# Optimization experiments

Measured on AMD Instinct MI355X. Metric: run time of the kernel, lower is better.

## Reference

```python
import jax, jax.numpy as jnp
import numpy as np

NUM_GROUPS = 8
EPS = 1e-5


def setup_inputs() -> dict:
    key = jax.random.key(0)
    ks = jax.random.split(key, 4)
    C = 128
    x = jax.random.normal(ks[0], (4, C, 64, 64), dtype=jnp.float32)
    gn_weight = jnp.ones((C,), dtype=jnp.float32)
    gn_bias = jnp.zeros((C,), dtype=jnp.float32)
    qkv_weight = jax.random.normal(ks[1], (3 * C, C), dtype=jnp.float32) * (C ** -0.5)
    qkv_bias = jnp.zeros((3 * C,), dtype=jnp.float32)
    proj_weight = jax.random.normal(ks[2], (C, C), dtype=jnp.float32) * (C ** -0.5)
    proj_bias = jnp.zeros((C,), dtype=jnp.float32)
    return {
        "x": x,
        "gn_weight": gn_weight,
        "gn_bias": gn_bias,
        "qkv_weight": qkv_weight,
        "qkv_bias": qkv_bias,
        "proj_weight": proj_weight,
        "proj_bias": proj_bias,
    }


def reference(x, gn_weight, gn_bias, qkv_weight, qkv_bias, proj_weight, proj_bias):
    b, c, h, w = x.shape
    scale = c ** (-0.5)

    # GroupNorm(8, c): normalize over (channels_in_group, h, w)
    xg = x.reshape(b, NUM_GROUPS, c // NUM_GROUPS, h, w)
    mean = jnp.mean(xg, axis=(2, 3, 4), keepdims=True)
    var = jnp.var(xg, axis=(2, 3, 4), keepdims=True)
    xn = ((xg - mean) * jax.lax.rsqrt(var + EPS)).reshape(b, c, h, w)
    xn = xn * gn_weight[None, :, None, None] + gn_bias[None, :, None, None]

    # 1x1 conv QKV == channel matmul; flatten spatial to sequence n = h*w
    xn_flat = xn.reshape(b, c, h * w)  # [b, c, n]
    qkv = jnp.einsum('oc,bcn->bno', qkv_weight, xn_flat) + qkv_bias  # [b, n, 3c]
    q, k, v = qkv[..., :c], qkv[..., c:2 * c], qkv[..., 2 * c:]

    # attention: materializes [b, n, n] scores as in original
    attn = jnp.einsum('bnc,bmc->bnm', q, k) * scale
    attn = jax.nn.softmax(attn, axis=-1)
    out = jnp.einsum('bnm,bmc->bnc', attn, v)  # [b, n, c]

    # proj 1x1 conv + residual
    out = jnp.einsum('oc,bnc->bno', proj_weight, out) + proj_bias  # [b, n, c]
    out = out.transpose(0, 2, 1).reshape(b, c, h, w)
    return x + out
```

## Files before the change

### kernel.cpp

```cpp
#include <hip/hip_runtime.h>

#define BATCH 4
#define CCH 128
#define NSP 4096
#define NGRP 8
#define GROUP_ELEMS 65536
#define QSCALE 0.12751744f
#define EPS_GN 1e-5f
#define OPSTRIDE 2097152
#define LPSTRIDE 16384

typedef short s8b __attribute__((ext_vector_type(8)));
typedef float f32x4 __attribute__((ext_vector_type(4)));

static __device__ __forceinline__ short f2bf(float f) {
  union { float f; unsigned u; } v; v.f = f;
  unsigned r = (v.u + 0x7FFFu + ((v.u >> 16) & 1u)) >> 16;
  return (short)r;
}

static __device__ __forceinline__ float bf2f(short s) {
  unsigned u = ((unsigned)(unsigned short)s) << 16;
  float f; __builtin_memcpy(&f, &u, 4); return f;
}

static __device__ __forceinline__ float fexp2(float x) {
#if __has_builtin(__builtin_amdgcn_exp2f)
  return __builtin_amdgcn_exp2f(x);
#else
  return exp2f(x);
#endif
}

static __device__ __forceinline__ unsigned pack2bf(float a, float b) {
  unsigned ua, ub;
  __builtin_memcpy(&ua, &a, 4); __builtin_memcpy(&ub, &b, 4);
  ua += 0x8000u; ub += 0x8000u;
#if __has_builtin(__builtin_amdgcn_perm)
  return __builtin_amdgcn_perm(ub, ua, 0x07060302u);
#else
  return (ua >> 16) | (ub & 0xFFFF0000u);
#endif
}

static __device__ __forceinline__ f32x4 mfma16(s8b a, s8b b, f32x4 c) {
  return __builtin_amdgcn_mfma_f32_16x16x32_bf16(a, b, c, 0, 0, 0);
}

static __device__ __forceinline__ void async16(const void* g, void* l) {
  __builtin_amdgcn_global_load_lds(
      (const __attribute__((address_space(1))) void*)g,
      (__attribute__((address_space(3))) void*)l, 16, 0, 0);
}

__global__ void gn_stats(const float* __restrict__ x, float* __restrict__ part) {
  int bx = blockIdx.x;
  int ch = bx & 7, bg = bx >> 3;
  const float* base = x + (size_t)bg * GROUP_ELEMS + (size_t)ch * 8192;
  int t = threadIdx.x;
  float s = 0.f, ss = 0.f;
  #pragma unroll
  for (int i = 0; i < 8; ++i) {
    float4 v = *(const float4*)(base + i * 1024 + t * 4);
    s  += v.x + v.y + v.z + v.w;
    ss += v.x * v.x + v.y * v.y + v.z * v.z + v.w * v.w;
  }
  #pragma unroll
  for (int off = 1; off < 64; off <<= 1) {
    s  += __shfl_xor(s, off);
    ss += __shfl_xor(ss, off);
  }
  __shared__ float red[8];
  int w = t >> 6;
  if ((t & 63) == 0) { red[w * 2] = s; red[w * 2 + 1] = ss; }
  __syncthreads();
  if (t == 0) {
    part[bx * 2]     = red[0] + red[2] + red[4] + red[6];
    part[bx * 2 + 1] = red[1] + red[3] + red[5] + red[7];
  }
}

__global__ void gn_apply(const float* __restrict__ x, const float* __restrict__ gw,
                         const float* __restrict__ gb, const float* __restrict__ part,
                         short* __restrict__ xn) {
  int bx = blockIdx.x;
  int ns = bx & 7, g = (bx >> 3) & 7, b = bx >> 6;
  int bg = b * NGRP + g;
  float s = 0.f, ss = 0.f;
  #pragma unroll
  for (int j = 0; j < 8; ++j) {
    s  += part[(bg * 8 + j) * 2];
    ss += part[(bg * 8 + j) * 2 + 1];
  }
  float mean = s * (1.f / GROUP_ELEMS);
  float var  = ss * (1.f / GROUP_ELEMS) - mean * mean;
  float inv  = rsqrtf(var + EPS_GN);
  int t = threadIdx.x;
  int cl = t & 15, n4 = t >> 4;
  int c = g * 16 + cl;
  float ga = gw[c] * inv;
  float be = gb[c] - mean * ga;
  const float* xr = x + (size_t)(b * CCH + c) * NSP;
  short* xo = xn + (size_t)b * NSP * CCH + c;
  #pragma unroll
  for (int i = 0; i < 8; ++i) {
    int n = ns * 512 + i * 64 + n4 * 4;
    float4 v = *(const float4*)(xr + n);
    xo[(size_t)(n + 0) * CCH] = f2bf(v.x * ga + be);
    xo[(size_t)(n + 1) * CCH] = f2bf(v.y * ga + be);
    xo[(size_t)(n + 2) * CCH] = f2bf(v.z * ga + be);
    xo[(size_t)(n + 3) * CCH] = f2bf(v.w * ga + be);
  }
}

__global__ void qkv_gemm(const short* __restrict__ xn, const float* __restrict__ Wqkv,
                         const float* __restrict__ bias, short* __restrict__ q,
                         short* __restrict__ k, short* __restrict__ vt) {
  __shared__ short Xl[128 * 136];
  __shared__ short Wl[64 * 136];
  int bx = blockIdx.x;
  int t = threadIdx.x;
  int lane = t & 63, w = t >> 6, l15 = lane & 15, quad = lane >> 4;
  if (bx < 1024) {
    int ot = bx & 3, nt = (bx >> 2) & 63, b = bx >> 8;
    for (int idx = t; idx < 64 * 16; idx += 256) {
      int row = idx >> 4, c8 = idx & 15;
      *(s8b*)&Xl[row * 136 + c8 * 8] =
          *(const s8b*)(xn + ((size_t)(b * NSP + nt * 64 + row)) * CCH + c8 * 8);
    }
    for (int idx = t; idx < 64 * 16; idx += 256) {
      int row = idx >> 4, c8 = idx & 15;
      const float* src = Wqkv + (size_t)(ot * 64 + row) * CCH + c8 * 8;
      s8b wv;
      #pragma unroll
      for (int j = 0; j < 8; ++j) wv[j] = f2bf(src[j]);
      *(s8b*)&Wl[row * 136 + c8 * 8] = wv;
    }
    __syncthreads();
    s8b a[4];
    #pragma unroll
    for (int kc = 0; kc < 4; ++kc)
      a[kc] = *(const s8b*)&Xl[(w * 16 + l15) * 136 + kc * 32 + quad * 8];
    #pragma unroll
    for (int o4 = 0; o4 < 4; ++o4) {
      f32x4 acc = {0.f, 0.f, 0.f, 0.f};
      #pragma unroll
      for (int kc = 0; kc < 4; ++kc) {
        s8b bw = *(const s8b*)&Wl[(o4 * 16 + l15) * 136 + kc * 32 + quad * 8];
        acc = mfma16(a[kc], bw, acc);
      }
      int obase = ot * 64 + o4 * 16;
      short* dst = (obase < 128) ? q : k;
      float mulf = (obase < 128) ? QSCALE : 1.0f;
      int oc = obase - ((obase < 128) ? 0 : 128) + l15;
      float bs = bias[obase + l15];
      #pragma unroll
      for (int r = 0; r < 4; ++r) {
        int n = nt * 64 + w * 16 + quad * 4 + r;
        dst[((size_t)(b * NSP + n)) * CCH + oc] = f2bf((acc[r] + bs) * mulf);
      }
    }
  } else {
    int vbx = bx - 1024;
    int ot = vbx & 1, nt = (vbx >> 1) & 31, b = vbx >> 6;
    for (int idx = t; idx < 128 * 16; idx += 256) {
      int row = idx >> 4, c8 = idx & 15;
      *(s8b*)&Xl[row * 136 + c8 * 8] =
          *(const s8b*)(xn + ((size_t)(b * NSP + nt * 128 + row)) * CCH + c8 * 8);
    }
    for (int idx = t; idx < 64 * 16; idx += 256) {
      int row = idx >> 4, c8 = idx & 15;
      const float* src = Wqkv + (size_t)(256 + ot * 64 + row) * CCH + c8 * 8;
      s8b wv;
      #pragma unroll
      for (int j = 0; j < 8; ++j) wv[j] = f2bf(src[j]);
      *(s8b*)&Wl[row * 136 + c8 * 8] = wv;
    }
    __syncthreads();
    s8b a[4];
    #pragma unroll
    for (int kc = 0; kc < 4; ++kc)
      a[kc] = *(const s8b*)&Wl[(w * 16 + l15) * 136 + kc * 32 + quad * 8];
    float bs[4];
    #pragma unroll
    for (int r = 0; r < 4; ++r) bs[r] = bias[256 + ot * 64 + w * 16 + quad * 4 + r];
    #pragma unroll
    for (int ntile = 0; ntile < 8; ++ntile) {
      f32x4 acc = {0.f, 0.f, 0.f, 0.f};
      #pragma unroll
      for (int kc = 0; kc < 4; ++kc) {
        s8b bx2 = *(const s8b*)&Xl[(ntile * 16 + l15) * 136 + kc * 32 + quad * 8];
        acc = mfma16(a[kc], bx2, acc);
      }
      int g2 = ntile & 3;
      int npos = nt * 128 + (ntile >> 2) * 64 + l15 * 2 + (g2 & 1) + 32 * (g2 >> 1);
      #pragma unroll
      for (int r = 0; r < 4; ++r) {
        int og = ot * 64 + w * 16 + quad * 4 + r;
        vt[((size_t)(b * CCH + og)) * NSP + npos] = f2bf(acc[r] + bs[r]);
      }
    }
  }
}

__global__ __launch_bounds__(256, 2) void flash(const short* __restrict__ q,
                                                const short* __restrict__ k,
                                                const short* __restrict__ vt,
                                                short* __restrict__ Op,
                                                float* __restrict__ Lp) {
  int bx = blockIdx.x;
  int kh = bx & 3, b = (bx >> 2) & 3, qt = bx >> 4;
  __shared__ short Kl[2][64 * 128];
  __shared__ short Vl[2][128 * 64];
  __shared__ short Pl[4][16 * 72];
  int t = threadIdx.x;
  int lane = t & 63, w = t >> 6;
  int l15 = lane & 15, quad = lane >> 4;
  const short* kbase = k + (size_t)b * NSP * CCH;
  const short* vbase = vt + (size_t)b * CCH * NSP;
  int kt0 = kh * 1024;

  int krow_in_chunk = lane >> 4, kgrp = lane & 15;
  int vrow_in_chunk = lane >> 3, vgrp = lane & 7;

  s8b aq[2][4];
  #pragma unroll
  for (int mt = 0; mt < 2; ++mt) {
    const short* qp =
        q + ((size_t)(b * NSP + qt * 128 + w * 32 + mt * 16 + l15)) * CCH + quad * 8;
    #pragma unroll
    for (int kc = 0; kc < 4; ++kc) aq[mt][kc] = *(const s8b*)(qp + kc * 32);
  }
  f32x4 O[2][8];
  f32x4 L[2];
  #pragma unroll
  for (int mt = 0; mt < 2; ++mt) {
    #pragma unroll
    for (int cg = 0; cg < 8; ++cg) O[mt][cg] = (f32x4){0.f, 0.f, 0.f, 0.f};
    L[mt] = (f32x4){0.f, 0.f, 0.f, 0.f};
  }
  s8b vone;
  #pragma unroll
  for (int j = 0; j < 8; ++j) vone[j] = (short)0x3F80;
  short* pw = &Pl[w][0];

  #define STAGE(buf_, key0_)                                                        \
    {                                                                               \
      const int key0v = (key0_);                                                    \
      _Pragma("unroll") for (int si = 0; si < 4; ++si) {                            \
        int c = w * 4 + si;                                                         \
        int rt = c * 4 + krow_in_chunk;                                             \
        async16(kbase + (size_t)(key0v + rt) * CCH + ((kgrp ^ (rt & 15)) * 8),      \
                &Kl[buf_][c * 512]);                                                \
        int rc = c * 8 + vrow_in_chunk;                                             \
        async16(vbase + (size_t)rc * NSP + key0v + ((vgrp ^ (rc & 7)) * 8),         \
                &Vl[buf_][c * 512]);                                                \
      }                                                                             \
    }

  STAGE(0, kt0)
  __syncthreads();

  for (int i = 0; i < 16; ++i) {
    int buf = i & 1;
    if (i < 15) STAGE(buf ^ 1, kt0 + (i + 1) * 64)

    f32x4 s[2][4];
    #pragma unroll
    for (int g2 = 0; g2 < 4; ++g2) {
      const short* kp = &Kl[buf][(g2 * 16 + l15) * 128];
      s8b bk[4];
      #pragma unroll
      for (int kc = 0; kc < 4; ++kc)
        bk[kc] = *(const s8b*)&kp[((kc * 4 + quad) ^ l15) * 8];
      #pragma unroll
      for (int mt = 0; mt < 2; ++mt) {
        f32x4 acc = {0.f, 0.f, 0.f, 0.f};
        acc = mfma16(aq[mt][0], bk[0], acc);
        acc = mfma16(aq[mt][1], bk[1], acc);
        acc = mfma16(aq[mt][2], bk[2], acc);
        acc = mfma16(aq[mt][3], bk[3], acc);
        s[mt][g2] = acc;
      }
    }
    s8b vf[8][2];
    #pragma unroll
    for (int cg = 0; cg < 8; ++cg) {
      const short* vp = &Vl[buf][(cg * 16 + l15) * 64];
      vf[cg][0] = *(const s8b*)&vp[((quad) ^ (l15 & 7)) * 8];
      vf[cg][1] = *(const s8b*)&vp[((4 + quad) ^ (l15 & 7)) * 8];
    }
    #pragma unroll
    for (int mt = 0; mt < 2; ++mt) {
      #pragma unroll
      for (int r = 0; r < 4; ++r) {
        float p0 = fexp2(s[mt][0][r]);
        float p1 = fexp2(s[mt][1][r]);
        float p2 = fexp2(s[mt][2][r]);
        float p3 = fexp2(s[mt][3][r]);
        *(unsigned*)&pw[(quad * 4 + r) * 72 + l15 * 2]      = pack2bf(p0, p1);
        *(unsigned*)&pw[(quad * 4 + r) * 72 + 32 + l15 * 2] = pack2bf(p2, p3);
      }
      s8b pf0 = *(const s8b*)&pw[l15 * 72 + quad * 8];
      s8b pf1 = *(const s8b*)&pw[l15 * 72 + 32 + quad * 8];
      L[mt] = mfma16(pf0, vone, L[mt]);
      L[mt] = mfma16(pf1, vone, L[mt]);
      #pragma unroll
      for (int cg = 0; cg < 8; ++cg) {
        O[mt][cg] = mfma16(pf0, vf[cg][0], O[mt][cg]);
        O[mt][cg] = mfma16(pf1, vf[cg][1], O[mt][cg]);
      }
    }
    __syncthreads();
  }

  short* ob = Op + (size_t)kh * OPSTRIDE + ((size_t)(b * NSP + qt * 128)) * CCH;
  float* lp = Lp + kh * LPSTRIDE + b * NSP + qt * 128;
  #pragma unroll
  for (int mt = 0; mt < 2; ++mt) {
    #pragma unroll
    for (int r = 0; r < 4; ++r) {
      int n = w * 32 + mt * 16 + quad * 4 + r;
      if (l15 == 0) lp[n] = L[mt][r];
      #pragma unroll
      for (int cg = 0; cg < 8; ++cg)
        ob[(size_t)n * CCH + cg * 16 + l15] = f2bf(O[mt][cg][r]);
    }
  }
}

__global__ void proj_gemm(const short* __restrict__ Op, const float* __restrict__ Lp,
                          const float* __restrict__ Wp, const float* __restrict__ pbias,
                          const float* __restrict__ x, float* __restrict__ out) {
  int bx = blockIdx.x;
  int nt = bx & 63, b = bx >> 6;
  __shared__ short Wl[128][136];
  int t = threadIdx.x;
  for (int idx = t; idx < 128 * 16; idx += 256) {
    int row = idx >> 4, c8 = idx & 15;
    const float* src = Wp + (size_t)row * CCH + c8 * 8;
    s8b wv;
    #pragma unroll
    for (int j = 0; j < 8; ++j) wv[j] = f2bf(src[j]);
    *(s8b*)&Wl[row][c8 * 8] = wv;
  }
  __syncthreads();
  int lane = t & 63, w = t >> 6, l15 = lane & 15, quad = lane >> 4;
  int row = nt * 64 + w * 16 + l15;
  float lsum = Lp[0 * LPSTRIDE + b * NSP + row] + Lp[1 * LPSTRIDE + b * NSP + row] +
               Lp[2 * LPSTRIDE + b * NSP + row] + Lp[3 * LPSTRIDE + b * NSP + row];
  float linv = 1.f / lsum;
  const short* ap = Op + ((size_t)(b * NSP + row)) * CCH + quad * 8;
  s8b bfr[4];
  #pragma unroll
  for (int kc = 0; kc < 4; ++kc) {
    float acc8[8];
    #pragma unroll
    for (int j = 0; j < 8; ++j) acc8[j] = 0.f;
    #pragma unroll
    for (int s = 0; s < 4; ++s) {
      s8b tv = *(const s8b*)(ap + (size_t)s * OPSTRIDE + kc * 32);
      #pragma unroll
      for (int j = 0; j < 8; ++j) acc8[j] += bf2f(tv[j]);
    }
    #pragma unroll
    for (int j = 0; j < 8; ++j) bfr[kc][j] = f2bf(acc8[j] * linv);
  }
  #pragma unroll
  for (int cg = 0; cg < 8; ++cg) {
    f32x4 acc = {0.f, 0.f, 0.f, 0.f};
    #pragma unroll
    for (int kc = 0; kc < 4; ++kc) {
      s8b aw = *(const s8b*)&Wl[cg * 16 + l15][kc * 32 + quad * 8];
      acc = mfma16(aw, bfr[kc], acc);
    }
    #pragma unroll
    for (int r = 0; r < 4; ++r) {
      int co = cg * 16 + quad * 4 + r;
      int n = nt * 64 + w * 16 + l15;
      size_t off = ((size_t)(b * CCH + co)) * NSP + n;
      out[off] = x[off] + acc[r] + pbias[co];
    }
  }
}

extern "C" void kernel_launch(void* const* d_in, const int* in_sizes, int n_in,
                              void* d_out, int out_size, void* d_ws, size_t ws_size,
                              hipStream_t stream) {
  (void)in_sizes; (void)n_in; (void)out_size; (void)ws_size;
  const float* x    = (const float*)d_in[0];
  const float* gw   = (const float*)d_in[1];
  const float* gb   = (const float*)d_in[2];
  const float* Wqkv = (const float*)d_in[3];
  const float* bqkv = (const float*)d_in[4];
  const float* Wp   = (const float*)d_in[5];
  const float* bp   = (const float*)d_in[6];
  float* out = (float*)d_out;
  char* ws = (char*)d_ws;
  float* part = (float*)ws;
  short* xn    = (short*)(ws + 4096);
  short* q     = (short*)(ws + 4096 + 1ull * 4194304);
  short* k     = (short*)(ws + 4096 + 2ull * 4194304);
  short* vt    = (short*)(ws + 4096 + 3ull * 4194304);
  short* Opart = (short*)(ws + 4096 + 4ull * 4194304);
  float* Lpart = (float*)(ws + 4096 + 8ull * 4194304);

  gn_stats<<<256, 256, 0, stream>>>(x, part);
  gn_apply<<<256, 256, 0, stream>>>(x, gw, gb, part, xn);
  qkv_gemm<<<1280, 256, 0, stream>>>(xn, Wqkv, bqkv, q, k, vt);
  flash<<<512, 256, 0, stream>>>(q, k, vt, Opart, Lpart);
  proj_gemm<<<256, 256, 0, stream>>>(Opart, Lpart, Wp, bp, x, out);
}
```

Before: 135.6 us.

## Enlarge flash query tile to 512 rows with 8 waves and 8-way key split

The flash kernel now runs 512-thread blocks, each covering 512 query rows (64 per wave, four 16-row m-tiles) over a 512-key slice, so the key range is split eight ways instead of four. Each staged K/V tile is reused across more query rows, which cuts LDS staging and global K/V traffic per unit of work. The P tile per wave grows to 64x72, so shared memory and accumulator registers rise (O becomes 4x8 f32x4). proj_gemm now reduces eight partial outputs and eight partial row sums instead of four, and Lpart moves to make room for the larger Opart buffer. The grid drops to 256 blocks, which may lower occupancy and adds split-reduction traffic in proj_gemm.

```diff
diff --git a/kernel.cpp b/kernel.cpp
--- a/kernel.cpp
+++ b/kernel.cpp
@@ -203,38 +203,38 @@
   }
 }
 
-__global__ __launch_bounds__(256, 2) void flash(const short* __restrict__ q,
-                                                const short* __restrict__ k,
-                                                const short* __restrict__ vt,
-                                                short* __restrict__ Op,
-                                                float* __restrict__ Lp) {
+__global__ __launch_bounds__(512) void flash(const short* __restrict__ q,
+                                             const short* __restrict__ k,
+                                             const short* __restrict__ vt,
+                                             short* __restrict__ Op,
+                                             float* __restrict__ Lp) {
   int bx = blockIdx.x;
-  int kh = bx & 3, b = (bx >> 2) & 3, qt = bx >> 4;
+  int kh = bx & 7, b = (bx >> 3) & 3, qt = bx >> 5;
   __shared__ short Kl[2][64 * 128];
   __shared__ short Vl[2][128 * 64];
-  __shared__ short Pl[4][16 * 72];
+  __shared__ short Pl[8][64 * 72];
   int t = threadIdx.x;
   int lane = t & 63, w = t >> 6;
   int l15 = lane & 15, quad = lane >> 4;
   const short* kbase = k + (size_t)b * NSP * CCH;
   const short* vbase = vt + (size_t)b * CCH * NSP;
-  int kt0 = kh * 1024;
+  int kt0 = kh * 512;
 
   int krow_in_chunk = lane >> 4, kgrp = lane & 15;
   int vrow_in_chunk = lane >> 3, vgrp = lane & 7;
 
-  s8b aq[2][4];
-  #pragma unroll
-  for (int mt = 0; mt < 2; ++mt) {
+  s8b aq[4][4];
+  #pragma unroll
+  for (int mt = 0; mt < 4; ++mt) {
     const short* qp =
-        q + ((size_t)(b * NSP + qt * 128 + w * 32 + mt * 16 + l15)) * CCH + quad * 8;
+        q + ((size_t)(b * NSP + qt * 512 + w * 64 + mt * 16 + l15)) * CCH + quad * 8;
     #pragma unroll
     for (int kc = 0; kc < 4; ++kc) aq[mt][kc] = *(const s8b*)(qp + kc * 32);
   }
-  f32x4 O[2][8];
-  f32x4 L[2];
-  #pragma unroll
-  for (int mt = 0; mt < 2; ++mt) {
+  f32x4 O[4][8];
+  f32x4 L[4];
+  #pragma unroll
+  for (int mt = 0; mt < 4; ++mt) {
     #pragma unroll
     for (int cg = 0; cg < 8; ++cg) O[mt][cg] = (f32x4){0.f, 0.f, 0.f, 0.f};
     L[mt] = (f32x4){0.f, 0.f, 0.f, 0.f};
@@ -247,8 +247,8 @@
   #define STAGE(buf_, key0_)                                                        \
     {                                                                               \
       const int key0v = (key0_);                                                    \
-      _Pragma("unroll") for (int si = 0; si < 4; ++si) {                            \
-        int c = w * 4 + si;                                                         \
+      _Pragma("unroll") for (int si = 0; si < 2; ++si) {                            \
+        int c = w * 2 + si;                                                         \
         int rt = c * 4 + krow_in_chunk;                                             \
         async16(kbase + (size_t)(key0v + rt) * CCH + ((kgrp ^ (rt & 15)) * 8),      \
                 &Kl[buf_][c * 512]);                                                \
@@ -261,66 +261,69 @@
   STAGE(0, kt0)
   __syncthreads();
 
-  for (int i = 0; i < 16; ++i) {
+  for (int i = 0; i < 8; ++i) {
     int buf = i & 1;
-    if (i < 15) STAGE(buf ^ 1, kt0 + (i + 1) * 64)
-
-    f32x4 s[2][4];
-    #pragma unroll
-    for (int g2 = 0; g2 < 4; ++g2) {
-      const short* kp = &Kl[buf][(g2 * 16 + l15) * 128];
-      s8b bk[4];
-      #pragma unroll
-      for (int kc = 0; kc < 4; ++kc)
-        bk[kc] = *(const s8b*)&kp[((kc * 4 + quad) ^ l15) * 8];
-      #pragma unroll
-      for (int mt = 0; mt < 2; ++mt) {
-        f32x4 acc = {0.f, 0.f, 0.f, 0.f};
-        acc = mfma16(aq[mt][0], bk[0], acc);
-        acc = mfma16(aq[mt][1], bk[1], acc);
-        acc = mfma16(aq[mt][2], bk[2], acc);
-        acc = mfma16(aq[mt][3], bk[3], acc);
-        s[mt][g2] = acc;
-      }
-    }
-    s8b vf[8][2];
+    if (i < 7) STAGE(buf ^ 1, kt0 + (i + 1) * 64)
+
+    #pragma unroll
+    for (int p = 0; p < 2; ++p) {
+      const short* kpa = &Kl[buf][((2 * p) * 16 + l15) * 128];
+      const short* kpb = &Kl[buf][((2 * p + 1) * 16 + l15) * 128];
+      s8b bka[4], bkb[4];
+      #pragma unroll
+      for (int kc = 0; kc < 4; ++kc) {
+        bka[kc] = *(const s8b*)&kpa[((kc * 4 + quad) ^ l15) * 8];
+        bkb[kc] = *(const s8b*)&kpb[((kc * 4 + quad) ^ l15) * 8];
+      }
+      #pragma unroll
+      for (int mt = 0; mt < 4; ++mt) {
+        f32x4 sa = {0.f, 0.f, 0.f, 0.f};
+        f32x4 sb = {0.f, 0.f, 0.f, 0.f};
+        #pragma unroll
+        for (int kc = 0; kc < 4; ++kc) sa = mfma16(aq[mt][kc], bka[kc], sa);
+        #pragma unroll
+        for (int kc = 0; kc < 4; ++kc) sb = mfma16(aq[mt][kc], bkb[kc], sb);
+        #pragma unroll
+        for (int r = 0; r < 4; ++r) {
+          float p0 = fexp2(sa[r]);
+          float p1 = fexp2(sb[r]);
+          *(unsigned*)&pw[(mt * 16 + quad * 4 + r) * 72 + p * 32 + l15 * 2] =
+              pack2bf(p0, p1);
+        }
+      }
+    }
+    s8b pf[4][2];
+    #pragma unroll
+    for (int mt = 0; mt < 4; ++mt) {
+      pf[mt][0] = *(const s8b*)&pw[(mt * 16 + l15) * 72 + quad * 8];
+      pf[mt][1] = *(const s8b*)&pw[(mt * 16 + l15) * 72 + 32 + quad * 8];
+    }
+    #pragma unroll
+    for (int mt = 0; mt < 4; ++mt) {
+      L[mt] = mfma16(pf[mt][0], vone, L[mt]);
+      L[mt] = mfma16(pf[mt][1], vone, L[mt]);
+    }
     #pragma unroll
     for (int cg = 0; cg < 8; ++cg) {
       const short* vp = &Vl[buf][(cg * 16 + l15) * 64];
-      vf[cg][0] = *(const s8b*)&vp[((quad) ^ (l15 & 7)) * 8];
-      vf[cg][1] = *(const s8b*)&vp[((4 + quad) ^ (l15 & 7)) * 8];
-    }
-    #pragma unroll
-    for (int mt = 0; mt < 2; ++mt) {
-      #pragma unroll
-      for (int r = 0; r < 4; ++r) {
-        float p0 = fexp2(s[mt][0][r]);
-        float p1 = fexp2(s[mt][1][r]);
-        float p2 = fexp2(s[mt][2][r]);
-        float p3 = fexp2(s[mt][3][r]);
-        *(unsigned*)&pw[(quad * 4 + r) * 72 + l15 * 2]      = pack2bf(p0, p1);
-        *(unsigned*)&pw[(quad * 4 + r) * 72 + 32 + l15 * 2] = pack2bf(p2, p3);
-      }
-      s8b pf0 = *(const s8b*)&pw[l15 * 72 + quad * 8];
-      s8b pf1 = *(const s8b*)&pw[l15 * 72 + 32 + quad * 8];
-      L[mt] = mfma16(pf0, vone, L[mt]);
-      L[mt] = mfma16(pf1, vone, L[mt]);
-      #pragma unroll
-      for (int cg = 0; cg < 8; ++cg) {
-        O[mt][cg] = mfma16(pf0, vf[cg][0], O[mt][cg]);
-        O[mt][cg] = mfma16(pf1, vf[cg][1], O[mt][cg]);
+      s8b vf0 = *(const s8b*)&vp[((quad) ^ (l15 & 7)) * 8];
+      s8b vf1 = *(const s8b*)&vp[((4 + quad) ^ (l15 & 7)) * 8];
+      #pragma unroll
+      for (int mt = 0; mt < 4; ++mt) {
+        O[mt][cg] = mfma16(pf[mt][0], vf0, O[mt][cg]);
+        O[mt][cg] = mfma16(pf[mt][1], vf1, O[mt][cg]);
       }
     }
     __syncthreads();
   }
 
-  short* ob = Op + (size_t)kh * OPSTRIDE + ((size_t)(b * NSP + qt * 128)) * CCH;
-  float* lp = Lp + kh * LPSTRIDE + b * NSP + qt * 128;
-  #pragma unroll
-  for (int mt = 0; mt < 2; ++mt) {
+  short* ob = Op + (size_t)kh * OPSTRIDE + ((size_t)(b * NSP + qt * 512)) * CCH;
+  float* lp = Lp + kh * LPSTRIDE + b * NSP + qt * 512;
+  #pragma unroll
+  for (int mt = 0; mt < 4; ++mt) {
     #pragma unroll
     for (int r = 0; r < 4; ++r) {
-      int n = w * 32 + mt * 16 + quad * 4 + r;
+      int n = w * 64 + mt * 16 + quad * 4 + r;
       if (l15 == 0) lp[n] = L[mt][r];
       #pragma unroll
       for (int cg = 0; cg < 8; ++cg)
@@ -347,8 +350,9 @@
   __syncthreads();
   int lane = t & 63, w = t >> 6, l15 = lane & 15, quad = lane >> 4;
   int row = nt * 64 + w * 16 + l15;
-  float lsum = Lp[0 * LPSTRIDE + b * NSP + row] + Lp[1 * LPSTRIDE + b * NSP + row] +
-               Lp[2 * LPSTRIDE + b * NSP + row] + Lp[3 * LPSTRIDE + b * NSP + row];
+  float lsum = 0.f;
+  #pragma unroll
+  for (int s = 0; s < 8; ++s) lsum += Lp[s * LPSTRIDE + b * NSP + row];
   float linv = 1.f / lsum;
   const short* ap = Op + ((size_t)(b * NSP + row)) * CCH + quad * 8;
   s8b bfr[4];
@@ -358,7 +362,7 @@
     #pragma unroll
     for (int j = 0; j < 8; ++j) acc8[j] = 0.f;
     #pragma unroll
-    for (int s = 0; s < 4; ++s) {
+    for (int s = 0; s < 8; ++s) {
       s8b tv = *(const s8b*)(ap + (size_t)s * OPSTRIDE + kc * 32);
       #pragma unroll
       for (int j = 0; j < 8; ++j) acc8[j] += bf2f(tv[j]);
@@ -403,11 +407,11 @@
   short* k     = (short*)(ws + 4096 + 2ull * 4194304);
   short* vt    = (short*)(ws + 4096 + 3ull * 4194304);
   short* Opart = (short*)(ws + 4096 + 4ull * 4194304);
-  float* Lpart = (float*)(ws + 4096 + 8ull * 4194304);
+  float* Lpart = (float*)(ws + 4096 + 12ull * 4194304);
 
   gn_stats<<<256, 256, 0, stream>>>(x, part);
   gn_apply<<<256, 256, 0, stream>>>(x, gw, gb, part, xn);
   qkv_gemm<<<1280, 256, 0, stream>>>(xn, Wqkv, bqkv, q, k, vt);
-  flash<<<512, 256, 0, stream>>>(q, k, vt, Opart, Lpart);
+  flash<<<256, 512, 0, stream>>>(q, k, vt, Opart, Lpart);
   proj_gemm<<<256, 256, 0, stream>>>(Opart, Lpart, Wp, bp, x, out);
 }
```

Measured after the change: 182.6 us. 1.35x slower.

## Use 32x32 MFMA with transposed S to keep P in registers in flash kernel

Applied to the files above, without the earlier changes.

Rewrites the flash attention inner loop to compute the transposed score tile with 32x32x16 bf16 MFMAs. The exponentiated probabilities are then packed directly into register operands for the PV MFMA, removing the per-wave LDS round trip for P and the extra MFMAs against a ones vector that computed row sums; row sums are now accumulated with scalar adds plus one cross-lane shuffle. The V^T store permutation in the QKV kernel is changed to match the new operand layout. The output is staged through LDS with a swizzle for coalesced 16-byte global stores, at the cost of more accumulator registers per thread.

```diff
diff --git a/kernel.cpp b/kernel.cpp
--- a/kernel.cpp
+++ b/kernel.cpp
@@ -12,6 +12,7 @@
 
 typedef short s8b __attribute__((ext_vector_type(8)));
 typedef float f32x4 __attribute__((ext_vector_type(4)));
+typedef float f32x16 __attribute__((ext_vector_type(16)));
 
 static __device__ __forceinline__ short f2bf(float f) {
   union { float f; unsigned u; } v; v.f = f;
@@ -43,8 +44,19 @@
 #endif
 }
 
+static __device__ __forceinline__ s8b pack8(float a0, float a1, float a2, float a3,
+                                            float a4, float a5, float a6, float a7) {
+  union { unsigned u[4]; s8b v; } x;
+  x.u[0] = pack2bf(a0, a1); x.u[1] = pack2bf(a2, a3);
+  x.u[2] = pack2bf(a4, a5); x.u[3] = pack2bf(a6, a7);
+  return x.v;
+}
+
 static __device__ __forceinline__ f32x4 mfma16(s8b a, s8b b, f32x4 c) {
   return __builtin_amdgcn_mfma_f32_16x16x32_bf16(a, b, c, 0, 0, 0);
+}
+static __device__ __forceinline__ f32x16 mfma32(s8b a, s8b b, f32x16 c) {
+  return __builtin_amdgcn_mfma_f32_32x32x16_bf16(a, b, c, 0, 0, 0);
 }
 
 static __device__ __forceinline__ void async16(const void* g, void* l) {
@@ -184,6 +196,7 @@
     float bs[4];
     #pragma unroll
     for (int r = 0; r < 4; ++r) bs[r] = bias[256 + ot * 64 + w * 16 + quad * 4 + r];
+    int ppos = 8 * ((l15 >> 2) & 1) + (l15 & 3) + 4 * (l15 >> 3);
     #pragma unroll
     for (int ntile = 0; ntile < 8; ++ntile) {
       f32x4 acc = {0.f, 0.f, 0.f, 0.f};
@@ -192,8 +205,7 @@
         s8b bx2 = *(const s8b*)&Xl[(ntile * 16 + l15) * 136 + kc * 32 + quad * 8];
         acc = mfma16(a[kc], bx2, acc);
       }
-      int g2 = ntile & 3;
-      int npos = nt * 128 + (ntile >> 2) * 64 + l15 * 2 + (g2 & 1) + 32 * (g2 >> 1);
+      int npos = nt * 128 + ntile * 16 + ppos;
       #pragma unroll
       for (int r = 0; r < 4; ++r) {
         int og = ot * 64 + w * 16 + quad * 4 + r;
@@ -212,10 +224,9 @@
   int kh = bx & 3, b = (bx >> 2) & 3, qt = bx >> 4;
   __shared__ short Kl[2][64 * 128];
   __shared__ short Vl[2][128 * 64];
-  __shared__ short Pl[4][16 * 72];
   int t = threadIdx.x;
   int lane = t & 63, w = t >> 6;
-  int l15 = lane & 15, quad = lane >> 4;
+  int l31 = lane & 31, h = lane >> 5;
   const short* kbase = k + (size_t)b * NSP * CCH;
   const short* vbase = vt + (size_t)b * CCH * NSP;
   int kt0 = kh * 1024;
@@ -223,26 +234,18 @@
   int krow_in_chunk = lane >> 4, kgrp = lane & 15;
   int vrow_in_chunk = lane >> 3, vgrp = lane & 7;
 
-  s8b aq[2][4];
-  #pragma unroll
-  for (int mt = 0; mt < 2; ++mt) {
-    const short* qp =
-        q + ((size_t)(b * NSP + qt * 128 + w * 32 + mt * 16 + l15)) * CCH + quad * 8;
-    #pragma unroll
-    for (int kc = 0; kc < 4; ++kc) aq[mt][kc] = *(const s8b*)(qp + kc * 32);
-  }
-  f32x4 O[2][8];
-  f32x4 L[2];
-  #pragma unroll
-  for (int mt = 0; mt < 2; ++mt) {
-    #pragma unroll
-    for (int cg = 0; cg < 8; ++cg) O[mt][cg] = (f32x4){0.f, 0.f, 0.f, 0.f};
-    L[mt] = (f32x4){0.f, 0.f, 0.f, 0.f};
-  }
-  s8b vone;
-  #pragma unroll
-  for (int j = 0; j < 8; ++j) vone[j] = (short)0x3F80;
-  short* pw = &Pl[w][0];
+  s8b aq[8];
+  {
+    const short* qp = q + ((size_t)(b * NSP + qt * 128 + w * 32 + l31)) * CCH + h * 8;
+    #pragma unroll
+    for (int kc = 0; kc < 8; ++kc) aq[kc] = *(const s8b*)(qp + kc * 16);
+  }
+  f32x16 O[4];
+  #pragma unroll
+  for (int cg = 0; cg < 4; ++cg)
+    #pragma unroll
+    for (int r = 0; r < 16; ++r) O[cg][r] = 0.f;
+  float lsum = 0.f;
 
   #define STAGE(buf_, key0_)                                                        \
     {                                                                               \
@@ -265,67 +268,60 @@
     int buf = i & 1;
     if (i < 15) STAGE(buf ^ 1, kt0 + (i + 1) * 64)
 
-    f32x4 s[2][4];
-    #pragma unroll
-    for (int g2 = 0; g2 < 4; ++g2) {
-      const short* kp = &Kl[buf][(g2 * 16 + l15) * 128];
-      s8b bk[4];
-      #pragma unroll
-      for (int kc = 0; kc < 4; ++kc)
-        bk[kc] = *(const s8b*)&kp[((kc * 4 + quad) ^ l15) * 8];
-      #pragma unroll
-      for (int mt = 0; mt < 2; ++mt) {
-        f32x4 acc = {0.f, 0.f, 0.f, 0.f};
-        acc = mfma16(aq[mt][0], bk[0], acc);
-        acc = mfma16(aq[mt][1], bk[1], acc);
-        acc = mfma16(aq[mt][2], bk[2], acc);
-        acc = mfma16(aq[mt][3], bk[3], acc);
-        s[mt][g2] = acc;
-      }
-    }
-    s8b vf[8][2];
-    #pragma unroll
-    for (int cg = 0; cg < 8; ++cg) {
-      const short* vp = &Vl[buf][(cg * 16 + l15) * 64];
-      vf[cg][0] = *(const s8b*)&vp[((quad) ^ (l15 & 7)) * 8];
-      vf[cg][1] = *(const s8b*)&vp[((4 + quad) ^ (l15 & 7)) * 8];
-    }
-    #pragma unroll
-    for (int mt = 0; mt < 2; ++mt) {
-      #pragma unroll
-      for (int r = 0; r < 4; ++r) {
-        float p0 = fexp2(s[mt][0][r]);
-        float p1 = fexp2(s[mt][1][r]);
-        float p2 = fexp2(s[mt][2][r]);
-        float p3 = fexp2(s[mt][3][r]);
-        *(unsigned*)&pw[(quad * 4 + r) * 72 + l15 * 2]      = pack2bf(p0, p1);
-        *(unsigned*)&pw[(quad * 4 + r) * 72 + 32 + l15 * 2] = pack2bf(p2, p3);
-      }
-      s8b pf0 = *(const s8b*)&pw[l15 * 72 + quad * 8];
-      s8b pf1 = *(const s8b*)&pw[l15 * 72 + 32 + quad * 8];
-      L[mt] = mfma16(pf0, vone, L[mt]);
-      L[mt] = mfma16(pf1, vone, L[mt]);
-      #pragma unroll
-      for (int cg = 0; cg < 8; ++cg) {
-        O[mt][cg] = mfma16(pf0, vf[cg][0], O[mt][cg]);
-        O[mt][cg] = mfma16(pf1, vf[cg][1], O[mt][cg]);
+    s8b pb[4];
+    #pragma unroll
+    for (int tile = 0; tile < 2; ++tile) {
+      f32x16 st;
+      #pragma unroll
+      for (int r = 0; r < 16; ++r) st[r] = 0.f;
+      const short* kp = &Kl[buf][(tile * 32 + l31) * 128];
+      #pragma unroll
+      for (int kc = 0; kc < 8; ++kc) {
+        s8b ak = *(const s8b*)&kp[(((kc * 2 + h) ^ (l31 & 15))) * 8];
+        st = mfma32(ak, aq[kc], st);
+      }
+      float pp[16];
+      #pragma unroll
+      for (int r = 0; r < 16; ++r) pp[r] = fexp2(st[r]);
+      lsum += (((pp[0] + pp[1]) + (pp[2] + pp[3])) + ((pp[4] + pp[5]) + (pp[6] + pp[7]))) +
+              (((pp[8] + pp[9]) + (pp[10] + pp[11])) + ((pp[12] + pp[13]) + (pp[14] + pp[15])));
+      pb[tile * 2 + 0] = pack8(pp[0], pp[1], pp[2], pp[3], pp[4], pp[5], pp[6], pp[7]);
+      pb[tile * 2 + 1] = pack8(pp[8], pp[9], pp[10], pp[11], pp[12], pp[13], pp[14], pp[15]);
+    }
+    #pragma unroll
+    for (int cg = 0; cg < 4; ++cg) {
+      const short* vp = &Vl[buf][(cg * 32 + l31) * 64];
+      #pragma unroll
+      for (int kc2 = 0; kc2 < 4; ++kc2) {
+        s8b av = *(const s8b*)&vp[(((kc2 * 2 + h) ^ (l31 & 7))) * 8];
+        O[cg] = mfma32(av, pb[kc2], O[cg]);
       }
     }
     __syncthreads();
   }
 
+  lsum += __shfl_xor(lsum, 32);
+
+  short* eb = &Kl[0][0] + w * 4096;
+  #pragma unroll
+  for (int cg = 0; cg < 4; ++cg)
+    #pragma unroll
+    for (int rp = 0; rp < 8; ++rp) {
+      int r = rp * 2;
+      int chlo = (r & 3) + 4 * h;
+      int chhi = cg * 4 + (r >> 2);
+      *(unsigned*)&eb[l31 * 128 + ((chhi ^ (l31 & 7))) * 8 + chlo] =
+          pack2bf(O[cg][r], O[cg][r + 1]);
+    }
   short* ob = Op + (size_t)kh * OPSTRIDE + ((size_t)(b * NSP + qt * 128)) * CCH;
   float* lp = Lp + kh * LPSTRIDE + b * NSP + qt * 128;
-  #pragma unroll
-  for (int mt = 0; mt < 2; ++mt) {
-    #pragma unroll
-    for (int r = 0; r < 4; ++r) {
-      int n = w * 32 + mt * 16 + quad * 4 + r;
-      if (l15 == 0) lp[n] = L[mt][r];
-      #pragma unroll
-      for (int cg = 0; cg < 8; ++cg)
-        ob[(size_t)n * CCH + cg * 16 + l15] = f2bf(O[mt][cg][r]);
-    }
+  if (lane < 32) lp[w * 32 + l31] = lsum;
+  __syncthreads();
+  for (int idx = t; idx < 128 * 16; idx += 256) {
+    int row = idx >> 4, c8 = idx & 15;
+    int w2 = row >> 5, nl = row & 31;
+    *(s8b*)(ob + (size_t)row * CCH + c8 * 8) =
+        *(const s8b*)(&Kl[0][0] + w2 * 4096 + nl * 128 + ((c8 ^ (nl & 7))) * 8);
   }
 }
 
```

Result: no change. 134.5 us (-0.8%).
